# Performance work log

Hardware: AMD Instinct MI355X
Metric: run time of the kernel (lower is better)

## Reference

```python
import jax, jax.numpy as jnp
import numpy as np

NEG = -9999.0      # chart init / clip floor (np.clip a_min=-9999.0)
THRESH = -9000.0   # 'pseudo_score > -9000' acceptance gate
ARC_BONUS = 5.0    # '+ 5' added to every arc candidate


def _fill_chart(vinfo):
    """Eisner DP chart fill, faithful to the sequential numpy triple loop.
    vinfo: [N, N] arc scores. Returns (score_chart [N,N,2,2], backtrace [N,N,2,2]).
    Chart axes: [i, j, direction, completeness] as in the torch source.
    Parallelized over span start i and split q; sequential over width k via scan.
    Sequential-update subtleties of the original q-loop are reproduced exactly:
      * complete (0,1) at q=i reads the (0,0) cell as it stands after only the
        q=i incomplete update ('part00');
      * complete (1,1) at q=j reads the fully updated (1,0) cell ('new10');
      * complete (0,1) at q=j and (1,1) at q=i are strict-improvement no-ops;
      * ties keep the earliest q (jnp.argmax returns first occurrence).
    """
    N = vinfo.shape[0]
    idx = jnp.arange(N)
    ii = idx[:, None]   # span start i
    mm = idx[None, :]   # split offset m; q = i + m
    S = jnp.full((N, N, 2, 2), NEG, dtype=vinfo.dtype).at[idx, idx].set(0.0)
    BT = jnp.zeros((N, N, 2, 2), dtype=jnp.int32)

    def step(carry, k):
        S, BT = carry
        j = idx + k
        row_ok = j < N
        okb = row_ok[:, None]
        jc = jnp.minimum(j, N - 1)
        jb = jc[:, None]
        q = ii + mm
        qc = jnp.minimum(q, N - 1)
        q1c = jnp.minimum(q + 1, N - 1)

        # ---- incomplete spans (0,0) and (1,0): q in [i, j-1]  <=>  m in [0, k-1]
        base = jnp.where((mm < k) & okb,
                         S[:, :, 1, 1][ii, qc] + S[:, :, 0, 1][q1c, jb],
                         -jnp.inf)                      # [N (i), N (m)]
        vL = vinfo[jc, idx][:, None]   # vinfo[j, i] -> arc j<-...: head j
        vR = vinfo[idx, jc][:, None]   # vinfo[i, j]
        p00 = jnp.maximum(base + vL + ARC_BONUS, NEG)
        p10 = jnp.maximum(base + vR + ARC_BONUS, NEG)
        m00 = jnp.max(p00, axis=1); q00 = idx + jnp.argmax(p00, axis=1)
        m10 = jnp.max(p10, axis=1); q10 = idx + jnp.argmax(p10, axis=1)
        ok00 = row_ok & (m00 > THRESH)
        ok10 = row_ok & (m10 > THRESH)
        # chart[i,j,0,0] as it stands right after the q=i iteration
        part00 = jnp.where(row_ok & (p00[:, 0] > THRESH), p00[:, 0], NEG)
        new10 = jnp.where(ok10, m10, NEG)

        m_mid = (mm >= 1) & (mm < k) & okb
        # ---- complete (0,1): q=i uses partially built (0,0); q=j is a no-op
        c01 = jnp.where(m_mid, S[:, :, 0, 1][ii, qc] + S[:, :, 0, 0][qc, jb], -jnp.inf)
        c01 = c01.at[:, 0].set(jnp.where(row_ok, part00, -jnp.inf))
        p01 = jnp.maximum(c01, NEG)
        m01 = jnp.max(p01, axis=1); q01 = idx + jnp.argmax(p01, axis=1)
        ok01 = row_ok & (m01 > THRESH)

        # ---- complete (1,1): q=i is a no-op; q=j uses freshly updated (1,0)
        c11 = jnp.where(m_mid, S[:, :, 1, 0][ii, qc] + S[:, :, 1, 1][qc, jb], -jnp.inf)
        c11 = jnp.where((mm == k) & okb, new10[:, None], c11)
        p11 = jnp.maximum(c11, NEG)
        m11 = jnp.max(p11, axis=1); q11 = idx + jnp.argmax(p11, axis=1)
        ok11 = row_ok & (m11 > THRESH)

        def upd(S, BT, a, b, ok, val, qarg):
            S = S.at[idx, jc, a, b].set(jnp.where(ok, val, S[idx, jc, a, b]))
            BT = BT.at[idx, jc, a, b].set(
                jnp.where(ok, qarg, BT[idx, jc, a, b]).astype(jnp.int32))
            return S, BT

        S, BT = upd(S, BT, 0, 0, ok00, m00, q00)
        S, BT = upd(S, BT, 1, 0, ok10, m10, q10)
        S, BT = upd(S, BT, 0, 1, ok01, m01, q01)
        S, BT = upd(S, BT, 1, 1, ok11, m11, q11)
        return (S, BT), None

    (S, BT), _ = jax.lax.scan(step, (S, BT), jnp.arange(1, N))
    return S, BT


def setup_inputs() -> dict:
    key = jax.random.key(0)
    B, N = 64, 128
    b_vinfo_mtx = jax.random.normal(key, (B, N, N), dtype=jnp.float32)
    b_buffer_size = jnp.full((B,), N, dtype=jnp.int32)
    return {"b_vinfo_mtx": b_vinfo_mtx, "b_buffer_size": b_buffer_size}


def reference(b_vinfo_mtx, b_buffer_size):
    # All sentences use the full buffer (b_buffer_size == N), so the batch is
    # processed as one vmapped chart fill.
    scores, backtrace = jax.vmap(_fill_chart)(b_vinfo_mtx)
    return scores, backtrace
```

## Files before the change

### kernel.cpp

```cpp
#include <hip/hip_runtime.h>
#include <stdint.h>

static constexpr int kN = 128;
static constexpr int kTri = (kN * (kN - 1)) / 2;
static constexpr int kTriD = (kN * (kN + 1)) / 2;
static constexpr int kThreads = 768;
static constexpr float kNeg = -9999.0f;
static constexpr float kThresh = -9000.0f;
static constexpr float kArcBonus = 5.0f;
static constexpr int kDynLds = kTriD * 16;
static constexpr int kCMax = 10;

__device__ __forceinline__ int rowBase(int i) { return (i * (2 * kN - 1 - i)) / 2; }
__device__ __forceinline__ int colBaseD(int c) { return (c * (c + 1)) / 2; }

__device__ __forceinline__ void ldsBarrier() {
    asm volatile("s_waitcnt lgkmcnt(0)\n\ts_barrier" ::: "memory");
}

template <int CTRL>
__device__ __forceinline__ float dppMax(float x) {
    const int y = __builtin_amdgcn_update_dpp(__float_as_int(x), __float_as_int(x),
                                              CTRL, 0xF, 0xF, true);
    return fmaxf(x, __int_as_float(y));
}
template <int CTRL>
__device__ __forceinline__ int dppMinI(int x) {
    const int y = __builtin_amdgcn_update_dpp(x, x, CTRL, 0xF, 0xF, true);
    return (y < x) ? y : x;
}
template <int P>
__device__ __forceinline__ float grpMax(float x) {
    float r = dppMax<0xB1>(x);
    if constexpr (P >= 4) r = dppMax<0x4E>(r);
    if constexpr (P >= 8) r = dppMax<0x141>(r);
    if constexpr (P >= 16) r = dppMax<0x140>(r);
    return r;
}
template <int P>
__device__ __forceinline__ int grpMinI(int x) {
    int r = dppMinI<0xB1>(x);
    if constexpr (P >= 4) r = dppMinI<0x4E>(r);
    if constexpr (P >= 8) r = dppMinI<0x141>(r);
    if constexpr (P >= 16) r = dppMinI<0x140>(r);
    return r;
}

__device__ __forceinline__ float4 writeCell(float4* __restrict__ Q4,
                                            uint32_t* __restrict__ wsBT,
                                            int qjb, int i, int wsIdx, int k,
                                            float gb, int ib, float vLc, float vRc,
                                            float v01, int i01, float v11, int i11) {
    const float v00 = (gb + vLc) + kArcBonus;
    const float v10 = (gb + vRc) + kArcBonus;
    const float new10 = (v10 > kThresh) ? v10 : kNeg;
    if (new10 > v11) { v11 = new10; i11 = k; }
    float4 w = make_float4(kNeg, kNeg, kNeg, kNeg);
    uint32_t p = 0;
    if (v00 > kThresh) { w.x = v00; p |= (uint32_t)(i + ib); }
    if (v01 > kThresh) { w.z = v01; p |= (uint32_t)(i + i01) << 8; }
    if (v10 > kThresh) { w.w = v10; p |= (uint32_t)(i + ib) << 16; }
    if (v11 > kThresh) { w.y = v11; p |= (uint32_t)(i + i11) << 24; }
    Q4[qjb + i] = w;
    wsBT[wsIdx] = p;
    return w;
}

__device__ __forceinline__ void doStepSerialReg(int k, int i,
                                                float4* __restrict__ Q4,
                                                uint32_t* __restrict__ wsBT,
                                                int& j, int& qjb, int rbi,
                                                const float*& pL, const float*& pR,
                                                float& vL, float& vR,
                                                float (&sr11)[17], float (&sr01)[17],
                                                float (&sr10)[17]) {
    const bool act = i < kN - k;
    const float vLc = vL, vRc = vR;
    const int qjbc = qjb;
    float bmax = -3.0e38f, v01 = -3.0e38f, v11 = -3.0e38f;
    int ib = 0, i01 = 0, i11 = 0x7FFFFFFF;
    if (act) {
        float4 cur = Q4[qjbc + i + 1];
        bmax = cur.z; ib = 0;
        const float p00 = (cur.z + vLc) + kArcBonus;
        v01 = (p00 > kThresh) ? p00 : kNeg; i01 = 0;
#pragma unroll
        for (int m = 1; m < 16; ++m) {
            if (m < k) {
                const float4 nxt = Q4[qjbc + i + m + 1];
                const float base = sr11[m] + nxt.z;
                const float p01v = sr01[m] + cur.x;
                const float p11v = sr10[m] + cur.y;
                if (base > bmax) { bmax = base; ib = m; }
                if (p01v > v01) { v01 = p01v; i01 = m; }
                if (p11v > v11) { v11 = p11v; i11 = m; }
                cur = nxt;
            }
        }
    }
    if (k < 16) {
        const bool nact = i < kN - (k + 1);
        qjb += j + 1; ++j; pL += kN; ++pR;
        vL = nact ? *pL : 0.f;
        vR = nact ? *pR : 0.f;
    }
    if (act) {
        const float4 w = writeCell(Q4, wsBT, qjbc, i, rbi + k - 1, k,
                                   bmax, ib, vLc, vRc, v01, i01, v11, i11);
        sr11[k] = w.y; sr01[k] = w.z; sr10[k] = w.w;
    }
}

template <int LP, int C>
__device__ __forceinline__ void preloadRow(int k0, int tid,
                                           const float4* __restrict__ Q4,
                                           float (&r11)[kCMax], float (&r01)[kCMax],
                                           float (&r10)[kCMax]) {
    const int i = tid >> LP;
    const int l = tid & ((1 << LP) - 1);
    const int mlo = l * C;
    const int mstart = mlo ? mlo : 1;
    const bool act = i < (kN - k0);
#pragma unroll
    for (int c = 0; c < C; ++c) {
        const int m = mstart + c;
        if (act && (m < mlo + C) && (m <= k0 - 1)) {
            const float4 d = Q4[colBaseD(i + m) + i];
            r11[c] = d.y; r01[c] = d.z; r10[c] = d.w;
        }
    }
}

template <int LP, int C>
__device__ __forceinline__ void fwInit(int k0, int tid,
                                       const float (&r11)[kCMax], const float (&r01)[kCMax],
                                       const float (&r10)[kCMax],
                                       float& fw11, float& fw01, float& fw10) {
    const int l = tid & ((1 << LP) - 1);
    const int mlo = l * C;
    const int mstart = mlo ? mlo : 1;
#pragma unroll
    for (int c = 0; c < C; ++c) {
        if (mstart + c == k0 - 1) { fw11 = r11[c]; fw01 = r01[c]; fw10 = r10[c]; }
    }
}

template <int LP, int C>
__device__ __forceinline__ void doStepC(int k, int i, int l,
                                        float4* __restrict__ Q4,
                                        uint32_t* __restrict__ wsBT,
                                        int& j, int& qjb, int rbi,
                                        const float*& pL, const float*& pR,
                                        float& vL, float& vR,
                                        float (&r11)[kCMax], float (&r01)[kCMax],
                                        float (&r10)[kCMax],
                                        float& fw11, float& fw01, float& fw10) {
    constexpr int P = 1 << LP;
    static_assert(P <= 16, "reductions must stay pure-DPP");
    const bool act = i < kN - k;
    const float vLc = vL, vRc = vR;
    const int mlo = l * C;
    const int mstart = mlo ? mlo : 1;
    const int mhi = (mlo + C < k) ? (mlo + C) : k;
    const int qjbc = qjb;

    float bmax = -3.0e38f, v01 = -3.0e38f, v11 = -3.0e38f;
    int ib = 0x7FFFFFFF, i01 = 0x7FFFFFFF, i11 = 0x7FFFFFFF;

    const int mf = k - 1;
    const bool lact = act && (mstart < mhi);
    float4 cur = make_float4(0.f, 0.f, 0.f, 0.f);
    if (lact) cur = Q4[qjbc + i + mstart];
    if (act && mlo == 0) {
        bmax = cur.z; ib = 0;
        const float p00 = (cur.z + vLc) + kArcBonus;
        v01 = (p00 > kThresh) ? p00 : kNeg; i01 = 0;
    }
#pragma unroll
    for (int c = 0; c < C; ++c) {
        const int m = mstart + c;
        const bool isF = (m == mf);
        const float a11 = isF ? fw11 : r11[c];
        const float a01 = isF ? fw01 : r01[c];
        const float a10 = isF ? fw10 : r10[c];
        r11[c] = a11; r01[c] = a01; r10[c] = a10;
        const bool on = lact && (m < mhi);
        if (on) {
            const float4 nxt = Q4[qjbc + i + m + 1];
            const float base = a11 + nxt.z;
            const float p01v = a01 + cur.x;
            const float p11v = a10 + cur.y;
            if (base > bmax) { bmax = base; ib = m; }
            if (p01v > v01) { v01 = p01v; i01 = m; }
            if (p11v > v11) { v11 = p11v; i11 = m; }
            cur = nxt;
        }
    }

    {
        const bool nact = i < kN - (k + 1);
        qjb += j + 1; ++j; pL += kN; ++pR;
        vL = nact ? *pL : 0.f;
        vR = nact ? *pR : 0.f;
    }

    const float gB = grpMax<P>(bmax);
    const float g01 = grpMax<P>(v01);
    const float g11 = grpMax<P>(v11);
    int cB = (bmax == gB) ? ib : 0x7FFFFFFF;
    int c01 = (v01 == g01) ? i01 : 0x7FFFFFFF;
    int c11 = (v11 == g11) ? i11 : 0x7FFFFFFF;
    cB = grpMinI<P>(cB);
    c01 = grpMinI<P>(c01);
    c11 = grpMinI<P>(c11);

    const float v10f = (gB + vRc) + kArcBonus;
    const float new10 = (v10f > kThresh) ? v10f : kNeg;
    float v11m = g11;
    if (new10 > v11m) v11m = new10;
    fw11 = (v11m > kThresh) ? v11m : kNeg;
    fw01 = (g01 > kThresh) ? g01 : kNeg;
    fw10 = (v10f > kThresh) ? v10f : kNeg;

    if (act && l == 0) {
        writeCell(Q4, wsBT, qjbc, i, rbi + k - 1, k,
                  gB, cB, vLc, vRc, g01, c01, g11, c11);
    }
}

template <int LP, int C>
__device__ __forceinline__ void runPhaseC(int k0, int k1, int tid,
        float4* __restrict__ Q4, uint32_t* __restrict__ wsBT,
        const float* __restrict__ v,
        float (&r11)[kCMax], float (&r01)[kCMax], float (&r10)[kCMax]) {
    const int i = tid >> LP;
    const int l = tid & ((1 << LP) - 1);
    const int firstGroup = (tid & ~63) >> LP;
    int kEnd = kN - firstGroup;
    if (kEnd > k1) kEnd = k1;
    if (kEnd > k0) {
        int j = i + k0;
        int qjb = colBaseD(j);
        const int rbi = rowBase(i & (kN - 1));
        const float* pL = v + (size_t)j * kN + i;
        const float* pR = v + (size_t)i * kN + j;
        const bool a0 = i < kN - k0;
        float vL = a0 ? *pL : 0.f;
        float vR = a0 ? *pR : 0.f;
        preloadRow<LP, C>(k0, tid, Q4, r11, r01, r10);
        float fw11 = kNeg, fw01 = kNeg, fw10 = kNeg;
        fwInit<LP, C>(k0, tid, r11, r01, r10, fw11, fw01, fw10);
        for (int k = k0; k < kEnd; ++k) {
            doStepC<LP, C>(k, i, l, Q4, wsBT, j, qjb, rbi, pL, pR, vL, vR,
                           r11, r01, r10, fw11, fw01, fw10);
            ldsBarrier();
        }
        for (int k = kEnd; k < k1; ++k) ldsBarrier();
    } else {
        for (int k = k0; k < k1; ++k) ldsBarrier();
    }
}

__global__ __launch_bounds__(kThreads) void eisner_dp(
    const float* __restrict__ vinfo,
    float* __restrict__ outS,
    float* __restrict__ outBT,
    uint32_t* __restrict__ btPacked)
{
    extern __shared__ float4 Q4[];

    const int tid = threadIdx.x;
    const int b = blockIdx.x;
    const float* v = vinfo + (size_t)b * kN * kN;
    uint32_t* wsBT = btPacked + (size_t)b * kTri;

    const float4 zeroq = make_float4(0.f, 0.f, 0.f, 0.f);
    if (tid < kN) Q4[colBaseD(tid) + tid] = zeroq;
    __syncthreads();

    if ((tid & ~63) < kN - 1) {
        const int i = tid;
        float sr11[17], sr01[17], sr10[17];
        int j = i + 1;
        int qjb = colBaseD(j);
        const int rbi = rowBase(i & (kN - 1));
        const float* pL = v + (size_t)j * kN + i;
        const float* pR = v + (size_t)i * kN + j;
        const bool a0 = i < kN - 1;
        float vL = a0 ? *pL : 0.f;
        float vR = a0 ? *pR : 0.f;
#pragma unroll
        for (int k = 1; k <= 16; ++k) {
            doStepSerialReg(k, i, Q4, wsBT, j, qjb, rbi, pL, pR, vL, vR,
                            sr11, sr01, sr10);
            ldsBarrier();
        }
    } else {
#pragma unroll
        for (int k = 1; k <= 16; ++k) ldsBarrier();
    }

    float r11[kCMax], r01[kCMax], r10[kCMax];
#pragma unroll
    for (int c = 0; c < kCMax; ++c) { r11[c] = kNeg; r01[c] = kNeg; r10[c] = kNeg; }

    runPhaseC<2, 6>(17, 24, tid, Q4, wsBT, v, r11, r01, r10);
    runPhaseC<2, 8>(24, 32, tid, Q4, wsBT, v, r11, r01, r10);
    runPhaseC<3, 6>(32, 48, tid, Q4, wsBT, v, r11, r01, r10);
    runPhaseC<3, 8>(48, 64, tid, Q4, wsBT, v, r11, r01, r10);
    runPhaseC<3, 10>(64, 80, tid, Q4, wsBT, v, r11, r01, r10);
    runPhaseC<4, 6>(80, 96, tid, Q4, wsBT, v, r11, r01, r10);
    runPhaseC<4, 8>(96, 128, tid, Q4, wsBT, v, r11, r01, r10);

    __syncthreads();

    float4* gS4 = (float4*)(outS + (size_t)b * kN * kN * 4);
    float4* gB4 = (float4*)(outBT + (size_t)b * kN * kN * 4);
    const float4 negq = make_float4(kNeg, kNeg, kNeg, kNeg);
    for (int c = tid; c < kN * kN; c += kThreads) {
        const int i = c >> 7, j = c & (kN - 1);
        if (i < j) {
            const float4 q = Q4[colBaseD(j) + i];
            gS4[c] = make_float4(q.x, q.z, q.w, q.y);
            const uint32_t p = wsBT[rowBase(i) + (j - i - 1)];
            gB4[c] = make_float4((float)(p & 255u), (float)((p >> 8) & 255u),
                                 (float)((p >> 16) & 255u), (float)(p >> 24));
        } else if (i == j) {
            gS4[c] = zeroq;
            gB4[c] = zeroq;
        } else {
            gS4[c] = negq;
            gB4[c] = zeroq;
        }
    }
}

extern "C" void kernel_launch(void* const* d_in, const int* in_sizes, int n_in,
                              void* d_out, int out_size, void* d_ws, size_t ws_size,
                              hipStream_t stream) {
    (void)n_in; (void)out_size; (void)ws_size;
    const float* vinfo = (const float*)d_in[0];
    const int B = in_sizes[1];
    float* outS = (float*)d_out;
    float* outBT = outS + (size_t)B * kN * kN * 4;
    uint32_t* btPacked = (uint32_t*)d_ws;

    hipFuncSetAttribute(reinterpret_cast<const void*>(eisner_dp),
                        hipFuncAttributeMaxDynamicSharedMemorySize, kDynLds);

    eisner_dp<<<dim3(B), dim3(kThreads), kDynLds, stream>>>(vinfo, outS, outBT, btPacked);
}
```

Baseline: 239.2 us.

## Overlap rows per wavefront to run two DP widths per barrier

```diff
diff --git a/kernel.cpp b/kernel.cpp
--- a/kernel.cpp
+++ b/kernel.cpp
@@ -4,7 +4,7 @@
 static constexpr int kN = 128;
 static constexpr int kTri = (kN * (kN - 1)) / 2;
 static constexpr int kTriD = (kN * (kN + 1)) / 2;
-static constexpr int kThreads = 768;
+static constexpr int kThreads = 1024;
 static constexpr float kNeg = -9999.0f;
 static constexpr float kThresh = -9000.0f;
 static constexpr float kArcBonus = 5.0f;
@@ -112,12 +112,10 @@
 }
 
 template <int LP, int C>
-__device__ __forceinline__ void preloadRow(int k0, int tid,
-                                           const float4* __restrict__ Q4,
-                                           float (&r11)[kCMax], float (&r01)[kCMax],
-                                           float (&r10)[kCMax]) {
-    const int i = tid >> LP;
-    const int l = tid & ((1 << LP) - 1);
+__device__ __forceinline__ void preloadRowI(int k0, int i, int l,
+                                            const float4* __restrict__ Q4,
+                                            float (&r11)[kCMax], float (&r01)[kCMax],
+                                            float (&r10)[kCMax]) {
     const int mlo = l * C;
     const int mstart = mlo ? mlo : 1;
     const bool act = i < (kN - k0);
@@ -132,11 +130,10 @@
 }
 
 template <int LP, int C>
-__device__ __forceinline__ void fwInit(int k0, int tid,
-                                       const float (&r11)[kCMax], const float (&r01)[kCMax],
-                                       const float (&r10)[kCMax],
-                                       float& fw11, float& fw01, float& fw10) {
-    const int l = tid & ((1 << LP) - 1);
+__device__ __forceinline__ void fwInitL(int k0, int l,
+                                        const float (&r11)[kCMax], const float (&r01)[kCMax],
+                                        const float (&r10)[kCMax],
+                                        float& fw11, float& fw01, float& fw10) {
     const int mlo = l * C;
     const int mstart = mlo ? mlo : 1;
 #pragma unroll
@@ -145,8 +142,8 @@
     }
 }
 
-template <int LP, int C>
-__device__ __forceinline__ void doStepC(int k, int i, int l,
+template <int LP, int C, bool SECOND>
+__device__ __forceinline__ void doStepS(int k, int i, int l, bool dup, float4 f,
                                         float4* __restrict__ Q4,
                                         uint32_t* __restrict__ wsBT,
                                         int& j, int& qjb, int rbi,
@@ -170,7 +167,12 @@
     const int mf = k - 1;
     const bool lact = act && (mstart < mhi);
     float4 cur = make_float4(0.f, 0.f, 0.f, 0.f);
-    if (lact) cur = Q4[qjbc + i + mstart];
+    if constexpr (SECOND) {
+        if (mlo == 0) cur = f;
+        else if (lact) cur = Q4[qjbc + i + mstart];
+    } else {
+        if (lact) cur = Q4[qjbc + i + mstart];
+    }
     if (act && mlo == 0) {
         bmax = cur.z; ib = 0;
         const float p00 = (cur.z + vLc) + kArcBonus;
@@ -222,42 +224,66 @@
     fw01 = (g01 > kThresh) ? g01 : kNeg;
     fw10 = (v10f > kThresh) ? v10f : kNeg;
 
-    if (act && l == 0) {
+    const bool doWrite = SECOND ? (act && l == 0 && !dup) : (act && l == 0);
+    if (doWrite) {
         writeCell(Q4, wsBT, qjbc, i, rbi + k - 1, k,
                   gB, cB, vLc, vRc, g01, c01, g11, c11);
     }
 }
 
 template <int LP, int C>
-__device__ __forceinline__ void runPhaseC(int k0, int k1, int tid,
+__device__ __forceinline__ void runPhaseS(int k0, int k1, int tid,
         float4* __restrict__ Q4, uint32_t* __restrict__ wsBT,
         const float* __restrict__ v,
         float (&r11)[kCMax], float (&r01)[kCMax], float (&r10)[kCMax]) {
-    const int i = tid >> LP;
-    const int l = tid & ((1 << LP) - 1);
-    const int firstGroup = (tid & ~63) >> LP;
-    int kEnd = kN - firstGroup;
+    constexpr int P = 1 << LP;
+    constexpr int G = 64 >> LP;
+    const int w = tid >> 6;
+    const int g = (tid & 63) >> LP;
+    const int l = tid & (P - 1);
+    const int i = w * (G - 1) + g;
+    const bool dup = (g == G - 1);
+    const int firstRow = w * (G - 1);
+    int kEnd = kN - firstRow;
     if (kEnd > k1) kEnd = k1;
-    if (kEnd > k0) {
-        int j = i + k0;
-        int qjb = colBaseD(j);
-        const int rbi = rowBase(i & (kN - 1));
-        const float* pL = v + (size_t)j * kN + i;
-        const float* pR = v + (size_t)i * kN + j;
-        const bool a0 = i < kN - k0;
-        float vL = a0 ? *pL : 0.f;
-        float vR = a0 ? *pR : 0.f;
-        preloadRow<LP, C>(k0, tid, Q4, r11, r01, r10);
-        float fw11 = kNeg, fw01 = kNeg, fw10 = kNeg;
-        fwInit<LP, C>(k0, tid, r11, r01, r10, fw11, fw01, fw10);
-        for (int k = k0; k < kEnd; ++k) {
-            doStepC<LP, C>(k, i, l, Q4, wsBT, j, qjb, rbi, pL, pR, vL, vR,
-                           r11, r01, r10, fw11, fw01, fw10);
-            ldsBarrier();
-        }
-        for (int k = kEnd; k < k1; ++k) ldsBarrier();
-    } else {
-        for (int k = k0; k < k1; ++k) ldsBarrier();
+
+    int j = i + k0;
+    int qjb = colBaseD(j);
+    const int rbi = rowBase(i & (kN - 1));
+    const float* pL = v + (size_t)j * kN + i;
+    const float* pR = v + (size_t)i * kN + j;
+    const bool a0 = i < kN - k0;
+    float vL = a0 ? *pL : 0.f;
+    float vR = a0 ? *pR : 0.f;
+    preloadRowI<LP, C>(k0, i, l, Q4, r11, r01, r10);
+    float fw11 = kNeg, fw01 = kNeg, fw10 = kNeg;
+    fwInitL<LP, C>(k0, l, r11, r01, r10, fw11, fw01, fw10);
+
+    const float4 fz = make_float4(0.f, 0.f, 0.f, 0.f);
+    int ks = k0;
+    if ((k1 - k0) & 1) {
+        if (k0 < kEnd) {
+            doStepS<LP, C, false>(k0, i, l, dup, fz, Q4, wsBT, j, qjb, rbi,
+                                  pL, pR, vL, vR, r11, r01, r10, fw11, fw01, fw10);
+        }
+        ldsBarrier();
+        ks = k0 + 1;
+    }
+    for (int k = ks; k < k1; k += 2) {
+        if (k < kEnd) {
+            if (dup && (i + k <= kN)) {
+                const float4 q = Q4[colBaseD(i + k - 1) + i];
+                fw11 = q.y; fw01 = q.z; fw10 = q.w;
+            }
+            doStepS<LP, C, false>(k, i, l, dup, fz, Q4, wsBT, j, qjb, rbi,
+                                  pL, pR, vL, vR, r11, r01, r10, fw11, fw01, fw10);
+            asm volatile("" ::: "memory");
+            float4 f = fz;
+            if (l == 0 && (i < kN - (k + 1))) f = Q4[qjb + i + 1];
+            doStepS<LP, C, true>(k + 1, i, l, dup, f, Q4, wsBT, j, qjb, rbi,
+                                 pL, pR, vL, vR, r11, r01, r10, fw11, fw01, fw10);
+        }
+        ldsBarrier();
     }
 }
 
@@ -278,7 +304,7 @@
     if (tid < kN) Q4[colBaseD(tid) + tid] = zeroq;
     __syncthreads();
 
-    if ((tid & ~63) < kN - 1) {
+    {
         const int i = tid;
         float sr11[17], sr01[17], sr10[17];
         int j = i + 1;
@@ -295,22 +321,17 @@
                             sr11, sr01, sr10);
             ldsBarrier();
         }
-    } else {
-#pragma unroll
-        for (int k = 1; k <= 16; ++k) ldsBarrier();
     }
 
     float r11[kCMax], r01[kCMax], r10[kCMax];
 #pragma unroll
     for (int c = 0; c < kCMax; ++c) { r11[c] = kNeg; r01[c] = kNeg; r10[c] = kNeg; }
 
-    runPhaseC<2, 6>(17, 24, tid, Q4, wsBT, v, r11, r01, r10);
-    runPhaseC<2, 8>(24, 32, tid, Q4, wsBT, v, r11, r01, r10);
-    runPhaseC<3, 6>(32, 48, tid, Q4, wsBT, v, r11, r01, r10);
-    runPhaseC<3, 8>(48, 64, tid, Q4, wsBT, v, r11, r01, r10);
-    runPhaseC<3, 10>(64, 80, tid, Q4, wsBT, v, r11, r01, r10);
-    runPhaseC<4, 6>(80, 96, tid, Q4, wsBT, v, r11, r01, r10);
-    runPhaseC<4, 8>(96, 128, tid, Q4, wsBT, v, r11, r01, r10);
+    runPhaseS<3, 5>(17, 40, tid, Q4, wsBT, v, r11, r01, r10);
+    runPhaseS<3, 8>(40, 64, tid, Q4, wsBT, v, r11, r01, r10);
+    runPhaseS<3, 10>(64, 80, tid, Q4, wsBT, v, r11, r01, r10);
+    runPhaseS<4, 6>(80, 96, tid, Q4, wsBT, v, r11, r01, r10);
+    runPhaseS<4, 8>(96, 128, tid, Q4, wsBT, v, r11, r01, r10);
 
     __syncthreads();
 
```

New measurement: 245.0 us. 1.02x slower.

## Run early widths barrier-free in overlapping wave tiles and raise block size

Applied to the files above, without the earlier changes.

```diff
diff --git a/kernel.cpp b/kernel.cpp
--- a/kernel.cpp
+++ b/kernel.cpp
@@ -4,12 +4,13 @@
 static constexpr int kN = 128;
 static constexpr int kTri = (kN * (kN - 1)) / 2;
 static constexpr int kTriD = (kN * (kN + 1)) / 2;
-static constexpr int kThreads = 768;
+static constexpr int kThreads = 1024;
 static constexpr float kNeg = -9999.0f;
 static constexpr float kThresh = -9000.0f;
 static constexpr float kArcBonus = 5.0f;
 static constexpr int kDynLds = kTriD * 16;
-static constexpr int kCMax = 10;
+static constexpr int kCMax = 9;
+static constexpr int kSer = 24;
 
 __device__ __forceinline__ int rowBase(int i) { return (i * (2 * kN - 1 - i)) / 2; }
 __device__ __forceinline__ int colBaseD(int c) { return (c * (c + 1)) / 2; }
@@ -66,15 +67,15 @@
     return w;
 }
 
-__device__ __forceinline__ void doStepSerialReg(int k, int i,
-                                                float4* __restrict__ Q4,
-                                                uint32_t* __restrict__ wsBT,
-                                                int& j, int& qjb, int rbi,
-                                                const float*& pL, const float*& pR,
-                                                float& vL, float& vR,
-                                                float (&sr11)[17], float (&sr01)[17],
-                                                float (&sr10)[17]) {
-    const bool act = i < kN - k;
+__device__ __forceinline__ void doStepSerialNB(int k, int lam, int i,
+                                               float4* __restrict__ Q4,
+                                               uint32_t* __restrict__ wsBT,
+                                               int& j, int& qjb, int rbi,
+                                               const float*& pL, const float*& pR,
+                                               float& vL, float& vR,
+                                               float (&sr11)[kSer + 1], float (&sr01)[kSer + 1],
+                                               float (&sr10)[kSer + 1]) {
+    const bool act = (lam + k <= 63) && (i < kN - k);
     const float vLc = vL, vRc = vR;
     const int qjbc = qjb;
     float bmax = -3.0e38f, v01 = -3.0e38f, v11 = -3.0e38f;
@@ -85,7 +86,7 @@
         const float p00 = (cur.z + vLc) + kArcBonus;
         v01 = (p00 > kThresh) ? p00 : kNeg; i01 = 0;
 #pragma unroll
-        for (int m = 1; m < 16; ++m) {
+        for (int m = 1; m < kSer; ++m) {
             if (m < k) {
                 const float4 nxt = Q4[qjbc + i + m + 1];
                 const float base = sr11[m] + nxt.z;
@@ -98,8 +99,8 @@
             }
         }
     }
-    if (k < 16) {
-        const bool nact = i < kN - (k + 1);
+    if (k < kSer) {
+        const bool nact = (lam + k + 1 <= 63) && (i < kN - (k + 1));
         qjb += j + 1; ++j; pL += kN; ++pR;
         vL = nact ? *pL : 0.f;
         vR = nact ? *pR : 0.f;
@@ -235,29 +236,21 @@
         float (&r11)[kCMax], float (&r01)[kCMax], float (&r10)[kCMax]) {
     const int i = tid >> LP;
     const int l = tid & ((1 << LP) - 1);
-    const int firstGroup = (tid & ~63) >> LP;
-    int kEnd = kN - firstGroup;
-    if (kEnd > k1) kEnd = k1;
-    if (kEnd > k0) {
-        int j = i + k0;
-        int qjb = colBaseD(j);
-        const int rbi = rowBase(i & (kN - 1));
-        const float* pL = v + (size_t)j * kN + i;
-        const float* pR = v + (size_t)i * kN + j;
-        const bool a0 = i < kN - k0;
-        float vL = a0 ? *pL : 0.f;
-        float vR = a0 ? *pR : 0.f;
-        preloadRow<LP, C>(k0, tid, Q4, r11, r01, r10);
-        float fw11 = kNeg, fw01 = kNeg, fw10 = kNeg;
-        fwInit<LP, C>(k0, tid, r11, r01, r10, fw11, fw01, fw10);
-        for (int k = k0; k < kEnd; ++k) {
-            doStepC<LP, C>(k, i, l, Q4, wsBT, j, qjb, rbi, pL, pR, vL, vR,
-                           r11, r01, r10, fw11, fw01, fw10);
-            ldsBarrier();
-        }
-        for (int k = kEnd; k < k1; ++k) ldsBarrier();
-    } else {
-        for (int k = k0; k < k1; ++k) ldsBarrier();
+    int j = i + k0;
+    int qjb = colBaseD(j);
+    const int rbi = rowBase(i & (kN - 1));
+    const float* pL = v + (size_t)j * kN + i;
+    const float* pR = v + (size_t)i * kN + j;
+    const bool a0 = i < kN - k0;
+    float vL = a0 ? *pL : 0.f;
+    float vR = a0 ? *pR : 0.f;
+    preloadRow<LP, C>(k0, tid, Q4, r11, r01, r10);
+    float fw11 = kNeg, fw01 = kNeg, fw10 = kNeg;
+    fwInit<LP, C>(k0, tid, r11, r01, r10, fw11, fw01, fw10);
+    for (int k = k0; k < k1; ++k) {
+        doStepC<LP, C>(k, i, l, Q4, wsBT, j, qjb, rbi, pL, pR, vL, vR,
+                       r11, r01, r10, fw11, fw01, fw10);
+        ldsBarrier();
     }
 }
 
@@ -278,39 +271,40 @@
     if (tid < kN) Q4[colBaseD(tid) + tid] = zeroq;
     __syncthreads();
 
-    if ((tid & ~63) < kN - 1) {
-        const int i = tid;
-        float sr11[17], sr01[17], sr10[17];
+    if (tid < 4 * 64) {
+        const int w = tid >> 6;
+        const int lam = tid & 63;
+        const int i = 40 * w + lam;
+        const int ic = (i < kN) ? i : (kN - 1);
+        float sr11[kSer + 1], sr01[kSer + 1], sr10[kSer + 1];
         int j = i + 1;
-        int qjb = colBaseD(j);
-        const int rbi = rowBase(i & (kN - 1));
-        const float* pL = v + (size_t)j * kN + i;
-        const float* pR = v + (size_t)i * kN + j;
-        const bool a0 = i < kN - 1;
+        int qjb = colBaseD((ic + 1 < kN) ? ic + 1 : kN - 1);
+        if (i + 1 < kN) qjb = colBaseD(i + 1);
+        const int rbi = rowBase(ic);
+        const float* pL = v + (size_t)((i + 1 < kN) ? i + 1 : 0) * kN + ic;
+        const float* pR = v + (size_t)ic * kN + ((i + 1 < kN) ? i + 1 : 0);
+        const bool a0 = (lam + 1 <= 63) && (i < kN - 1);
         float vL = a0 ? *pL : 0.f;
         float vR = a0 ? *pR : 0.f;
 #pragma unroll
-        for (int k = 1; k <= 16; ++k) {
-            doStepSerialReg(k, i, Q4, wsBT, j, qjb, rbi, pL, pR, vL, vR,
-                            sr11, sr01, sr10);
-            ldsBarrier();
-        }
-    } else {
-#pragma unroll
-        for (int k = 1; k <= 16; ++k) ldsBarrier();
-    }
+        for (int k = 1; k <= kSer; ++k) {
+            doStepSerialNB(k, lam, i, Q4, wsBT, j, qjb, rbi, pL, pR, vL, vR,
+                           sr11, sr01, sr10);
+            asm volatile("" ::: "memory");
+        }
+    }
+    ldsBarrier();
 
     float r11[kCMax], r01[kCMax], r10[kCMax];
 #pragma unroll
     for (int c = 0; c < kCMax; ++c) { r11[c] = kNeg; r01[c] = kNeg; r10[c] = kNeg; }
 
-    runPhaseC<2, 6>(17, 24, tid, Q4, wsBT, v, r11, r01, r10);
-    runPhaseC<2, 8>(24, 32, tid, Q4, wsBT, v, r11, r01, r10);
-    runPhaseC<3, 6>(32, 48, tid, Q4, wsBT, v, r11, r01, r10);
-    runPhaseC<3, 8>(48, 64, tid, Q4, wsBT, v, r11, r01, r10);
-    runPhaseC<3, 10>(64, 80, tid, Q4, wsBT, v, r11, r01, r10);
-    runPhaseC<4, 6>(80, 96, tid, Q4, wsBT, v, r11, r01, r10);
-    runPhaseC<4, 8>(96, 128, tid, Q4, wsBT, v, r11, r01, r10);
+    runPhaseC<3, 5>(25, 40, tid, Q4, wsBT, v, r11, r01, r10);
+    runPhaseC<3, 7>(40, 56, tid, Q4, wsBT, v, r11, r01, r10);
+    runPhaseC<3, 9>(56, 64, tid, Q4, wsBT, v, r11, r01, r10);
+    runPhaseC<4, 5>(64, 80, tid, Q4, wsBT, v, r11, r01, r10);
+    runPhaseC<4, 7>(80, 112, tid, Q4, wsBT, v, r11, r01, r10);
+    runPhaseC<4, 9>(112, 128, tid, Q4, wsBT, v, r11, r01, r10);
 
     __syncthreads();
 
```

Result: faster. 228.1 us (-4.7%).
